# Kernel tuning notes

Hardware: AMD Instinct MI355X
Metric: run time of the kernel (lower is better)

## Reference

```python
import jax, jax.numpy as jnp
import numpy as np

DIM = 1024
NUM_HEADS = 16
HEAD_DIM = DIM // NUM_HEADS
B, T = 2, 2048


def setup_inputs() -> dict:
    key = jax.random.key(0)
    ks = jax.random.split(key, 7)
    x = jax.random.normal(ks[0], (B, T, DIM), dtype=jnp.float32)
    # causal mask, broadcastable over batch and heads
    mask = jnp.tril(jnp.ones((T, T), dtype=bool))[None, None, :, :]
    # rope tables for half rotary angles, tiled to head_dim (cat of two halves)
    pos = jnp.arange(T, dtype=jnp.float32)[:, None]
    inv_freq = 1.0 / (10000.0 ** (jnp.arange(0, HEAD_DIM, 2, dtype=jnp.float32) / HEAD_DIM))
    ang = pos * inv_freq[None, :]                      # [T, hd/2]
    ang = jnp.concatenate([ang, ang], axis=-1)         # [T, hd]
    rope_sin = jnp.sin(ang)[None, None, :, :]
    rope_cos = jnp.cos(ang)[None, None, :, :]
    s = 0.02
    qkv_w = jax.random.normal(ks[1], (DIM, 3 * DIM), dtype=jnp.float32) * s
    qkv_b = jnp.zeros((3 * DIM,), dtype=jnp.float32)
    proj_w = jax.random.normal(ks[2], (DIM, DIM), dtype=jnp.float32) * s
    proj_b = jnp.zeros((DIM,), dtype=jnp.float32)
    return {"x": x, "mask": mask, "rope_sin": rope_sin, "rope_cos": rope_cos,
            "qkv_w": qkv_w, "qkv_b": qkv_b, "proj_w": proj_w, "proj_b": proj_b}


def _rotate_half(t):
    half = t.shape[-1] // 2
    return jnp.concatenate([-t[..., half:], t[..., :half]], axis=-1)


def _apply_rope(t, sin, cos):
    return t * cos + _rotate_half(t) * sin


def reference(x, mask, rope_sin, rope_cos, qkv_w, qkv_b, proj_w, proj_b):
    Bb, Tt, C = x.shape
    qkv = x @ qkv_w + qkv_b                            # [B, T, 3C]
    q, k, v = jnp.split(qkv, 3, axis=-1)
    def split_heads(t):                                # [B, T, C] -> [B, H, T, hd]
        return t.reshape(Bb, Tt, NUM_HEADS, HEAD_DIM).transpose(0, 2, 1, 3)
    q, k, v = split_heads(q), split_heads(k), split_heads(v)
    sin = rope_sin[:, :, :Tt, :]
    cos = rope_cos[:, :, :Tt, :]
    q = _apply_rope(q, sin, cos)
    k = _apply_rope(k, sin, cos)
    att = jnp.einsum("bhqd,bhkd->bhqk", q, k) / (HEAD_DIM ** 0.5)
    att = jnp.where(mask, att, -jnp.inf)
    att = jax.nn.softmax(att, axis=-1)
    y = jnp.einsum("bhqk,bhkd->bhqd", att, v)          # [B, H, T, hd]
    y = y.transpose(0, 2, 1, 3).reshape(Bb, Tt, C)
    return y @ proj_w + proj_b
```

## Files before the change

### kernel.cpp

```cpp
#include <hip/hip_runtime.h>

typedef unsigned short u16;
typedef u16 u16x8 __attribute__((ext_vector_type(8)));
typedef __bf16 bf16x8 __attribute__((ext_vector_type(8)));
typedef float f32x4 __attribute__((ext_vector_type(4)));

#define T_SEQ 2048
#define DIM 1024
#define NH 16
#define HD 64

#define MFMA(a, b, c) __builtin_amdgcn_mfma_f32_16x16x32_bf16(a, b, c, 0, 0, 0)

__device__ __forceinline__ u16 f2bf(float f) {
  return __builtin_bit_cast(u16, static_cast<__bf16>(f));
}

__device__ __forceinline__ bf16x8 ld8(const u16* p) {
  return __builtin_bit_cast(bf16x8, *(const u16x8*)p);
}

__device__ __forceinline__ void gload_lds16(const u16* g, u16* l) {
  __builtin_amdgcn_global_load_lds((const __attribute__((address_space(1))) void*)(g),
                                   (__attribute__((address_space(3))) void*)(l),
                                   16, 0, 0);
}

__global__ void k_prep(const float* __restrict__ X, u16* __restrict__ Y,
                       const float* __restrict__ Wq, u16* __restrict__ WqT,
                       const float* __restrict__ Wp, u16* __restrict__ WpT) {
  __shared__ float tile[32][33];
  int bid = blockIdx.x;
  if (bid < 4096) {
    int i = (bid * 256 + threadIdx.x) * 4;
    float4 f = *(const float4*)&X[i];
    ushort4 o = make_ushort4(f2bf(f.x), f2bf(f.y), f2bf(f.z), f2bf(f.w));
    *(ushort4*)&Y[i] = o;
    return;
  }
  const float* W; u16* WT; int K = 1024, N, bx, by;
  if (bid < 4096 + 3072) { int t = bid - 4096; W = Wq; WT = WqT; N = 3072; bx = t % 96; by = t / 96; }
  else                   { int t = bid - 7168; W = Wp; WT = WpT; N = 1024; bx = t % 32; by = t / 32; }
  int tx = threadIdx.x & 31, ty = threadIdx.x >> 5;
  int c0 = bx * 32, r0 = by * 32;
#pragma unroll
  for (int r = 0; r < 4; r++)
    tile[ty + r * 8][tx] = W[(r0 + ty + r * 8) * N + c0 + tx];
  __syncthreads();
#pragma unroll
  for (int r = 0; r < 4; r++)
    WT[(c0 + ty + r * 8) * K + r0 + tx] = f2bf(tile[tx][ty + r * 8]);
}


#define GEMM_STAGE3(buf, kk)                                                      \
  {                                                                               \
    _Pragma("unroll") for (int p = 0; p < 2; p++) {                               \
      int rr = w * 32 + p * 16;                                                   \
      gload_lds16(&Agp[(size_t)(rowBase + rr + srow) * Kd + (kk) + schunk],       \
                  &As[buf][rr * 32]);                                             \
      gload_lds16(&Bgp[(size_t)(colBase + rr + srow) * Kd + (kk) + schunk],       \
                  &Bs[buf][rr * 32]);                                             \
    }                                                                             \
  }

#define GEMM_COMPUTE3(buf)                                                        \
  {                                                                               \
    bf16x8 af[4], bfv[4];                                                         \
    _Pragma("unroll") for (int i = 0; i < 4; i++) {                               \
      af[i] = ld8(&As[buf][(wm * 64 + i * 16 + l15) * 32 + quad * 8]);            \
      bfv[i] = ld8(&Bs[buf][(wn * 64 + i * 16 + l15) * 32 + quad * 8]);           \
    }                                                                             \
    _Pragma("unroll") for (int i = 0; i < 4; i++)                                 \
        _Pragma("unroll") for (int j = 0; j < 4; j++)                             \
            acc[i][j] = MFMA(af[i], bfv[j], acc[i][j]);                           \
  }

#define GEMM_CORE3(Aptr, BTptr, bxv, byv)                                         \
  const int tid = threadIdx.x;                                                    \
  const int lane = tid & 63, w = tid >> 6;                                        \
  const int l15 = lane & 15, quad = lane >> 4;                                    \
  const int wm = w >> 1, wn = w & 1;                                              \
  const int rowBase = (byv) * 128;                                                \
  const int colBase = (bxv) * 128;                                                \
  const u16* Agp = (Aptr);                                                        \
  const u16* Bgp = (BTptr);                                                       \
  const int Kd = DIM;                                                             \
  f32x4 acc[4][4];                                                                \
  _Pragma("unroll") for (int i = 0; i < 4; i++)                                   \
      _Pragma("unroll") for (int j = 0; j < 4; j++)                               \
          acc[i][j] = (f32x4){0.f, 0.f, 0.f, 0.f};                                \
  const int srow = lane >> 2;                 \
  const int schunk = (lane & 3) * 8;    \
  GEMM_STAGE3(0, 0)                                                               \
  GEMM_STAGE3(1, 32)                                                              \
  _Pragma("unroll") for (int s = 0; s < 32; ++s) {                                \
    if (s < 31) { asm volatile("s_waitcnt vmcnt(4)" ::: "memory"); }              \
    else        { asm volatile("s_waitcnt vmcnt(0)" ::: "memory"); }              \
    __builtin_amdgcn_s_barrier();                                                 \
    if (s + 2 < 32) { GEMM_STAGE3((s + 2) % 3, (s + 2) * 32) }                    \
    GEMM_COMPUTE3(s % 3)                                                          \
  }                                                                               \
  __syncthreads();

#define EPLD 136

__global__ __launch_bounds__(256) void k_gemm_qkv(
    const u16* __restrict__ A, const u16* __restrict__ BT,
    const float* __restrict__ bias,
    const float* __restrict__ rsin, const float* __restrict__ rcos,
    u16* __restrict__ qb, u16* __restrict__ kb, u16* __restrict__ vtb) {
  __shared__ __align__(16) u16 LDSBUF[24576];
  u16 (*As)[128 * 32] = (u16(*)[128 * 32])(LDSBUF);
  u16 (*Bs)[128 * 32] = (u16(*)[128 * 32])(LDSBUF + 12288);
  const int n = blockIdx.x, xcd = n & 7, s = n >> 3;
  const int cg = xcd & 1, rg = xcd >> 1;
  const int bxv = cg * 12 + (s >> 3);
  const int byv = rg * 8 + (s & 7);
  GEMM_CORE3(A, BT, bxv, byv)

#pragma unroll
  for (int j = 0; j < 4; j++) {
    float bv = bias[colBase + wn * 64 + j * 16 + l15];
#pragma unroll
    for (int i = 0; i < 4; i++)
#pragma unroll
      for (int r = 0; r < 4; r++) acc[i][j][r] += bv;
  }

  const int colW = colBase + wn * 64;
  const int sec = colW >> 10;

  if (sec == 2) {
#pragma unroll
    for (int i = 0; i < 4; i++)
#pragma unroll
      for (int r = 0; r < 4; r++) {
        int tl = wm * 64 + i * 16 + quad * 4 + r;
#pragma unroll
        for (int j = 0; j < 4; j++) {
          int d2 = wn * 64 + j * 16 + l15;
          LDSBUF[d2 * EPLD + tl] = f2bf(acc[i][j][r]);
        }
      }
  } else {
#pragma unroll
    for (int i = 0; i < 4; i++)
#pragma unroll
      for (int r = 0; r < 4; r++) {
        int tl = wm * 64 + i * 16 + quad * 4 + r;
        int t = (rowBase + tl) & 2047;
#pragma unroll
        for (int j = 0; j < 4; j++) {
          int d = j * 16 + l15;
          float v = acc[i][j][r];
          float pr = acc[i][j ^ 2][r];
          float rot = (j < 2) ? -pr : pr;
          float rv = v * rcos[t * HD + d] + rot * rsin[t * HD + d];
          if (sec == 0) rv *= 0.125f;
          LDSBUF[tl * EPLD + wn * 64 + d] = f2bf(rv);
        }
      }
  }
  __syncthreads();

  const int hb = (colBase & 1023) >> 6;
  const int b = rowBase >> 11, t0 = rowBase & 2047;
  if (sec == 2) {
#pragma unroll
    for (int p = 0; p < 8; p++) {
      int drow = (tid >> 4) + p * 16;
      int tc = (tid & 15) * 8;
      int hh = hb + (drow >> 6), d = drow & 63;
      u16x8 v = *(const u16x8*)&LDSBUF[drow * EPLD + tc];
      *(u16x8*)&vtb[((size_t)(b * NH + hh) * HD + d) * T_SEQ + t0 + tc] = v;
    }
  } else {
    u16* dst = (sec == 0) ? qb : kb;
#pragma unroll
    for (int p = 0; p < 8; p++) {
      int row = (tid >> 4) + p * 16;
      int dc = (tid & 15) * 8;
      int hh = hb + (dc >> 6), d = dc & 63;
      u16x8 v = *(const u16x8*)&LDSBUF[row * EPLD + dc];
      *(u16x8*)&dst[((size_t)(b * NH + hh) * T_SEQ + t0 + row) * HD + d] = v;
    }
  }
}

__global__ __launch_bounds__(256) void k_gemm_proj(
    const u16* __restrict__ A, const u16* __restrict__ BT,
    const float* __restrict__ bias, float* __restrict__ C) {
  __shared__ __align__(16) u16 LDSBUF[24576];
  u16 (*As)[128 * 32] = (u16(*)[128 * 32])(LDSBUF);
  u16 (*Bs)[128 * 32] = (u16(*)[128 * 32])(LDSBUF + 12288);
  const int n = blockIdx.x, xcd = n & 7, s = n >> 3;
  const int cg = xcd & 1, rg = xcd >> 1;
  const int bxv = cg * 4 + (s >> 3);
  const int byv = rg * 8 + (s & 7);
  GEMM_CORE3(A, BT, bxv, byv)

#pragma unroll
  for (int i = 0; i < 4; i++)
#pragma unroll
    for (int r = 0; r < 4; r++) {
      int grow = rowBase + wm * 64 + i * 16 + quad * 4 + r;
#pragma unroll
      for (int j = 0; j < 4; j++) {
        int col = colBase + wn * 64 + j * 16 + l15;
        C[grow * DIM + col] = acc[i][j][r] + bias[col];
      }
    }
}

#define KLD 72
#define VLD 136

__global__ __launch_bounds__(256, 3) void k_attn(
    const u16* __restrict__ qb, const u16* __restrict__ kb,
    const u16* __restrict__ vtb, u16* __restrict__ yb) {
  __shared__ __align__(16) u16 Ks[128 * KLD];
  __shared__ __align__(16) u16 VTs[64 * VLD];
  __shared__ __align__(16) u16 Ps[64 * VLD];
  const int tid = threadIdx.x;
  const int lane = tid & 63, w = tid >> 6;
  const int l15 = lane & 15, quad = lane >> 4;
  const int bh = blockIdx.x;
  const int qt = 31 - blockIdx.y;

  const u16* qp = qb + (size_t)bh * T_SEQ * HD;
  const u16* kp = kb + (size_t)bh * T_SEQ * HD;
  const u16* vp = vtb + (size_t)bh * HD * T_SEQ;

  const int nch = (qt + 2) >> 1;
  const int qrow_base = qt * 64 + w * 16 + quad * 4;

  const int sr = tid >> 3, sc = (tid & 7) * 8;
  const int vr = tid >> 4, vc = (tid & 15) * 8;

  u16x8 kreg[4], vreg[4];
#define LOADKV(c)                                                              \
  {                                                                            \
    _Pragma("unroll") for (int p = 0; p < 4; p++)                              \
        kreg[p] = *(const u16x8*)&kp[((c) * 128 + sr + p * 32) * HD + sc];     \
    _Pragma("unroll") for (int p = 0; p < 4; p++)                              \
        vreg[p] = *(const u16x8*)&vp[(vr + p * 16) * T_SEQ + (c) * 128 + vc];  \
  }
#define WRITEKV()                                                              \
  {                                                                            \
    _Pragma("unroll") for (int p = 0; p < 4; p++)                              \
        *(u16x8*)&Ks[(sr + p * 32) * KLD + sc] = kreg[p];                      \
    _Pragma("unroll") for (int p = 0; p < 4; p++)                              \
        *(u16x8*)&VTs[(vr + p * 16) * VLD + vc] = vreg[p];                     \
  }

  LOADKV(0)

  {
#pragma unroll
    for (int p = 0; p < 2; p++) {
      int r = sr + p * 32;
      *(u16x8*)&Ps[r * KLD + sc] = *(const u16x8*)&qp[(qt * 64 + r) * HD + sc];
    }
  }
  __syncthreads();
  bf16x8 qa0 = ld8(&Ps[(w * 16 + l15) * KLD + quad * 8]);
  bf16x8 qa1 = ld8(&Ps[(w * 16 + l15) * KLD + 32 + quad * 8]);
  WRITEKV()
  __syncthreads();

  f32x4 o[4];
#pragma unroll
  for (int j = 0; j < 4; j++) o[j] = (f32x4){0.f, 0.f, 0.f, 0.f};
  float li[4] = {0.f, 0.f, 0.f, 0.f};

  u16* ps = &Ps[w * 16 * VLD];
  const int srd = ((l15 & 1) << 3) | ((l15 >> 2) << 1) | ((l15 >> 1) & 1);

  for (int c = 0; c < nch; c++) {
    if (c + 1 < nch) LOADKV(c + 1)

    f32x4 s[8];
#pragma unroll
    for (int j = 0; j < 8; j++) {
      s[j] = (f32x4){0.f, 0.f, 0.f, 0.f};
      bf16x8 b0 = ld8(&Ks[(j * 16 + l15) * KLD + quad * 8]);
      bf16x8 b1 = ld8(&Ks[(j * 16 + l15) * KLD + 32 + quad * 8]);
      s[j] = MFMA(qa0, b0, s[j]);
      s[j] = MFMA(qa1, b1, s[j]);
    }

    const bool lastc = (c == nch - 1);
#pragma unroll
    for (int r = 0; r < 4; r++) {
      const int swr = ((r & 1) << 3) | (quad << 1) | (r >> 1);
#pragma unroll
      for (int j = 0; j < 8; j++) {
        float e = __expf(s[j][r]);
        if (lastc && (c * 128 + j * 16 + l15 > qrow_base + r)) e = 0.f;
        li[r] += e;
        ps[swr * VLD + j * 16 + l15] = f2bf(e);
      }
    }

#pragma unroll
    for (int c4 = 0; c4 < 4; c4++) {
      bf16x8 pa = ld8(&ps[srd * VLD + c4 * 32 + quad * 8]);
#pragma unroll
      for (int j2 = 0; j2 < 4; j2++) {
        bf16x8 vb = ld8(&VTs[(j2 * 16 + l15) * VLD + c4 * 32 + quad * 8]);
        o[j2] = MFMA(pa, vb, o[j2]);
      }
    }
    __syncthreads();
    if (c + 1 < nch) {
      WRITEKV()
      __syncthreads();
    }
  }

#pragma unroll
  for (int r = 0; r < 4; r++) {
#pragma unroll
    for (int off = 8; off >= 1; off >>= 1) li[r] += __shfl_xor(li[r], off, 16);
    li[r] = 1.0f / li[r];
  }

#pragma unroll
  for (int j = 0; j < 4; j++)
#pragma unroll
    for (int r = 0; r < 4; r++) {
      const int swr = ((r & 1) << 3) | (quad << 1) | (r >> 1);
      ps[swr * VLD + j * 16 + l15] = f2bf(o[j][r] * li[r]);
    }
  __syncthreads();

  const int b = bh >> 4, h = bh & 15;
  {
    int sr2 = tid >> 3, sc2 = (tid & 7) * 8;
#pragma unroll
    for (int p = 0; p < 2; p++) {
      int row = sr2 + p * 32;
      int m = row & 15;
      int srow = ((m & 1) << 3) | ((m >> 2) << 1) | ((m >> 1) & 1);
      int t = qt * 64 + row;
      *(u16x8*)&yb[((size_t)(b * T_SEQ + t) * NH + h) * HD + sc2] =
          *(const u16x8*)&Ps[((row & 48) | srow) * VLD + sc2];
    }
  }
}

extern "C" void kernel_launch(void* const* d_in, const int* in_sizes, int n_in,
                              void* d_out, int out_size, void* d_ws, size_t ws_size,
                              hipStream_t stream) {
  const float* x      = (const float*)d_in[0];
  const float* rsin   = (const float*)d_in[2];
  const float* rcos   = (const float*)d_in[3];
  const float* qkv_w  = (const float*)d_in[4];
  const float* qkv_b  = (const float*)d_in[5];
  const float* proj_w = (const float*)d_in[6];
  const float* proj_b = (const float*)d_in[7];
  float* out = (float*)d_out;

  char* ws = (char*)d_ws;
  u16* x_bf  = (u16*)(ws);
  u16* qkvT  = (u16*)(ws + (8ull << 20));
  u16* projT = (u16*)(ws + (14ull << 20));
  u16* q_buf = (u16*)(ws + (16ull << 20));
  u16* k_buf = (u16*)(ws + (24ull << 20));
  u16* vT    = (u16*)(ws + (32ull << 20));
  u16* y_buf = (u16*)(ws + (40ull << 20));

  hipLaunchKernelGGL(k_prep, dim3(8192), dim3(256), 0, stream,
                     x, x_bf, qkv_w, qkvT, proj_w, projT);
  hipLaunchKernelGGL(k_gemm_qkv, dim3(768), dim3(256), 0, stream,
                     x_bf, qkvT, qkv_b, rsin, rcos, q_buf, k_buf, vT);
  hipLaunchKernelGGL(k_attn, dim3(32, 32), dim3(256), 0, stream,
                     q_buf, k_buf, vT, y_buf);
  hipLaunchKernelGGL(k_gemm_proj, dim3(256), dim3(256), 0, stream,
                     y_buf, projT, proj_b, out);
}
```

Before: 188.2 us.

## Widen attention blocks to 128 query rows with eight waves sharing K/V tiles

The attention kernel now launches 512-thread blocks covering 128 query rows instead of 256-thread blocks covering 64, so each staged 128-key K/V tile in LDS serves twice as many query rows. The grid's query dimension is halved, the per-thread K/V staging loads drop from four to two vectors, and the Q staging, P scratch and output write-back are re-indexed for eight waves. This is meant to cut redundant global K/V reads and staging work per query row. In exchange it adds LDS use per block, makes causal work per block coarser, and lowers launch bounds to two blocks per CU.

```diff
diff --git a/kernel.cpp b/kernel.cpp
--- a/kernel.cpp
+++ b/kernel.cpp
@@ -216,42 +216,42 @@
 #define KLD 72
 #define VLD 136
 
-__global__ __launch_bounds__(256, 3) void k_attn(
+__global__ __launch_bounds__(512, 2) void k_attn(
     const u16* __restrict__ qb, const u16* __restrict__ kb,
     const u16* __restrict__ vtb, u16* __restrict__ yb) {
   __shared__ __align__(16) u16 Ks[128 * KLD];
   __shared__ __align__(16) u16 VTs[64 * VLD];
-  __shared__ __align__(16) u16 Ps[64 * VLD];
+  __shared__ __align__(16) u16 Ps[8 * 16 * VLD];
   const int tid = threadIdx.x;
   const int lane = tid & 63, w = tid >> 6;
   const int l15 = lane & 15, quad = lane >> 4;
   const int bh = blockIdx.x;
-  const int qt = 31 - blockIdx.y;
-
-  const u16* qp = qb + (size_t)bh * T_SEQ * HD;
+  const int qp = 15 - blockIdx.y;
+
+  const u16* qp_ = qb + (size_t)bh * T_SEQ * HD;
   const u16* kp = kb + (size_t)bh * T_SEQ * HD;
   const u16* vp = vtb + (size_t)bh * HD * T_SEQ;
 
-  const int nch = (qt + 2) >> 1;
-  const int qrow_base = qt * 64 + w * 16 + quad * 4;
-
-  const int sr = tid >> 3, sc = (tid & 7) * 8;
+  const int nch = qp + 1;
+  const int qrow_base = qp * 128 + w * 16 + quad * 4;
+
+  const int kr = tid >> 3, kc = (tid & 7) * 8;
   const int vr = tid >> 4, vc = (tid & 15) * 8;
 
-  u16x8 kreg[4], vreg[4];
+  u16x8 kreg[2], vreg[2];
 #define LOADKV(c)                                                              \
   {                                                                            \
-    _Pragma("unroll") for (int p = 0; p < 4; p++)                              \
-        kreg[p] = *(const u16x8*)&kp[((c) * 128 + sr + p * 32) * HD + sc];     \
-    _Pragma("unroll") for (int p = 0; p < 4; p++)                              \
-        vreg[p] = *(const u16x8*)&vp[(vr + p * 16) * T_SEQ + (c) * 128 + vc];  \
+    _Pragma("unroll") for (int p = 0; p < 2; p++)                              \
+        kreg[p] = *(const u16x8*)&kp[((c) * 128 + kr + p * 64) * HD + kc];     \
+    _Pragma("unroll") for (int p = 0; p < 2; p++)                              \
+        vreg[p] = *(const u16x8*)&vp[(vr + p * 32) * T_SEQ + (c) * 128 + vc];  \
   }
 #define WRITEKV()                                                              \
   {                                                                            \
-    _Pragma("unroll") for (int p = 0; p < 4; p++)                              \
-        *(u16x8*)&Ks[(sr + p * 32) * KLD + sc] = kreg[p];                      \
-    _Pragma("unroll") for (int p = 0; p < 4; p++)                              \
-        *(u16x8*)&VTs[(vr + p * 16) * VLD + vc] = vreg[p];                     \
+    _Pragma("unroll") for (int p = 0; p < 2; p++)                              \
+        *(u16x8*)&Ks[(kr + p * 64) * KLD + kc] = kreg[p];                      \
+    _Pragma("unroll") for (int p = 0; p < 2; p++)                              \
+        *(u16x8*)&VTs[(vr + p * 32) * VLD + vc] = vreg[p];                     \
   }
 
   LOADKV(0)
@@ -259,8 +259,8 @@
   {
 #pragma unroll
     for (int p = 0; p < 2; p++) {
-      int r = sr + p * 32;
-      *(u16x8*)&Ps[r * KLD + sc] = *(const u16x8*)&qp[(qt * 64 + r) * HD + sc];
+      int r = kr + p * 64;
+      *(u16x8*)&Ps[r * KLD + kc] = *(const u16x8*)&qp_[(qp * 128 + r) * HD + kc];
     }
   }
   __syncthreads();
@@ -336,17 +336,14 @@
   __syncthreads();
 
   const int b = bh >> 4, h = bh & 15;
-  {
-    int sr2 = tid >> 3, sc2 = (tid & 7) * 8;
-#pragma unroll
-    for (int p = 0; p < 2; p++) {
-      int row = sr2 + p * 32;
-      int m = row & 15;
-      int srow = ((m & 1) << 3) | ((m >> 2) << 1) | ((m >> 1) & 1);
-      int t = qt * 64 + row;
-      *(u16x8*)&yb[((size_t)(b * T_SEQ + t) * NH + h) * HD + sc2] =
-          *(const u16x8*)&Ps[((row & 48) | srow) * VLD + sc2];
-    }
+#pragma unroll
+  for (int p = 0; p < 2; p++) {
+    int row = kr + p * 64;
+    int m = row & 15;
+    int srow = ((m & 1) << 3) | ((m >> 2) << 1) | ((m >> 1) & 1);
+    int t = qp * 128 + row;
+    *(u16x8*)&yb[((size_t)(b * T_SEQ + t) * NH + h) * HD + kc] =
+        *(const u16x8*)&Ps[(((row >> 4) << 4) | srow) * VLD + kc];
   }
 }
 
@@ -375,7 +372,7 @@
                      x, x_bf, qkv_w, qkvT, proj_w, projT);
   hipLaunchKernelGGL(k_gemm_qkv, dim3(768), dim3(256), 0, stream,
                      x_bf, qkvT, qkv_b, rsin, rcos, q_buf, k_buf, vT);
-  hipLaunchKernelGGL(k_attn, dim3(32, 32), dim3(256), 0, stream,
+  hipLaunchKernelGGL(k_attn, dim3(32, 16), dim3(512), 0, stream,
                      q_buf, k_buf, vT, y_buf);
   hipLaunchKernelGGL(k_gemm_proj, dim3(256), dim3(256), 0, stream,
                      y_buf, projT, proj_b, out);
```

Measured after the change: 188.7 us. No clear change (+0.3%).
